# Performance work log

Hardware: AMD Instinct MI355X
Metric: run time of the kernel (lower is better)

Reference implementation:

```python
import jax, jax.numpy as jnp
import numpy as np


def setup_inputs() -> dict:
    key = jax.random.key(0)
    k1, k2, k3, k4 = jax.random.split(key, 4)
    B, S, E, A = 4, 4096, 1024, 1024
    embedded = jax.random.normal(k1, (B, S, E), dtype=jnp.float32)
    # nn.Linear(E, A, bias=False) weights, stored as [E, A] so y = x @ W
    Wk = jax.random.normal(k2, (E, A), dtype=jnp.float32) * (E ** -0.5)
    Wq = jax.random.normal(k3, (E, A), dtype=jnp.float32) * (E ** -0.5)
    Wv = jax.random.normal(k4, (E, A), dtype=jnp.float32) * (E ** -0.5)
    return {"embedded": embedded, "Wk": Wk, "Wq": Wq, "Wv": Wv}


def reference(embedded, Wk, Wq, Wv):
    # K, Q, V projections: [B, S, A]
    K = embedded @ Wk
    Q = embedded @ Wq
    V = embedded @ Wv
    A = K.shape[-1]
    S = embedded.shape[1]
    # causal scores [B, S, S]
    scores = jnp.einsum("bqa,bka->bqk", Q, K) / jnp.sqrt(jnp.float32(A))
    causal = jnp.tril(jnp.ones((S, S), dtype=bool))
    scores = jnp.where(causal, scores, -jnp.inf)
    probs = jax.nn.softmax(scores, axis=-1)
    out = jnp.einsum("bqk,bka->bqa", probs, V)
    # torch.round(out, decimals=4)
    return jnp.round(out, 4)
```

## Files before the change

### kernel.cpp

```cpp
#include <hip/hip_runtime.h>
#include <hip/hip_fp16.h>

typedef __attribute__((ext_vector_type(4))) float f32x4;
typedef __attribute__((ext_vector_type(8))) short s16x8;
typedef __attribute__((ext_vector_type(4))) short s16x4;
typedef unsigned short u16;
typedef unsigned int u32;

__device__ __forceinline__ u16 f2bf(float f) {
    union { float f; unsigned u; } x; x.f = f;
    return (u16)((x.u + 0x7fffu + ((x.u >> 16) & 1u)) >> 16);
}

__device__ __forceinline__ void ld16(const void* g, void* l) {
    __builtin_amdgcn_global_load_lds(
        (const __attribute__((address_space(1))) unsigned int*)g,
        (__attribute__((address_space(3))) unsigned int*)l, 16, 0, 0);
}

__device__ __forceinline__ void kstep64(const u16* gA, const u16* gB, const u16* gC,
                                        long lda, long ldb,
                                        u16* sA, u16* sB,
                                        int wm, int wn, int lm, int lg,
                                        f32x4 acc0[4][4], f32x4 acc1[4][4])
{
    const int t = threadIdx.x;
    __syncthreads();
#pragma unroll
    for (int p = 0; p < 4; p++) {
        ld16(gA + (long)p * 32 * lda, sA + p * 2048 + t * 8);
        ld16(gB + (long)p * 32 * ldb, sB + p * 2048 + t * 8);
        ld16(gC + (long)p * 32 * ldb, sB + 8192 + p * 2048 + t * 8);
    }
    __syncthreads();

#pragma unroll
    for (int s = 0; s < 2; s++) {
        s16x8 af[4], bf[4], cf[4];
        const int co = (((s * 4 + lg) ^ (lm & 7)) << 3);
#pragma unroll
        for (int i = 0; i < 4; i++) {
            af[i] = *(const s16x8*)&sA[(wm + i * 16 + lm) * 64 + co];
            bf[i] = *(const s16x8*)&sB[(wn + i * 16 + lm) * 64 + co];
            cf[i] = *(const s16x8*)&sB[8192 + (wn + i * 16 + lm) * 64 + co];
        }
#pragma unroll
        for (int i = 0; i < 4; i++)
#pragma unroll
            for (int j = 0; j < 4; j++) {
                acc0[i][j] = __builtin_amdgcn_mfma_f32_16x16x32_bf16(af[i], bf[j], acc0[i][j], 0, 0, 0);
                acc1[i][j] = __builtin_amdgcn_mfma_f32_16x16x32_bf16(af[i], cf[j], acc1[i][j], 0, 0, 0);
            }
    }
}

__device__ __forceinline__ void gemm_core64(const u16* A, long lda,
                                            const u16* B0, const u16* B1, long ldb,
                                            int m0, int kEnd,
                                            f32x4 acc0[4][4], f32x4 acc1[4][4],
                                            u16* sA, u16* sB)
{
    const int t    = threadIdx.x;
    const int lane = t & 63;
    const int wave = t >> 6;
    const int wm   = (wave & 1) << 6;
    const int wn   = (wave >> 1) << 6;
    const int lm   = lane & 15;
    const int lg   = lane >> 4;
    const int sr   = t >> 3;
    const int sc   = (((t & 7) ^ ((t >> 3) & 7)) << 3);
    const u16* gA0 = A + (long)(m0 + sr) * lda + sc;
    const u16* gB0 = B0 + (long)sr * ldb + sc;
    const u16* gC0 = B1 + (long)sr * ldb + sc;

    for (int k0 = 0; k0 < kEnd; k0 += 64)
        kstep64(gA0 + k0, gB0 + k0, gC0 + k0, lda, ldb,
                sA, sB, wm, wn, lm, lg, acc0, acc1);
}

__global__ void convert_x(const float* __restrict__ X, u16* __restrict__ Xb) {
    long idx = ((long)blockIdx.x * 256 + threadIdx.x) * 4;
    f32x4 v = *(const f32x4*)&X[idx];
    s16x4 o;
    o.x = (short)f2bf(v.x); o.y = (short)f2bf(v.y);
    o.z = (short)f2bf(v.z); o.w = (short)f2bf(v.w);
    *(s16x4*)&Xb[idx] = o;
}

__global__ void convert_w(const float* __restrict__ Wk, const float* __restrict__ Wq,
                          const float* __restrict__ Wv,
                          u16* __restrict__ Wkt, u16* __restrict__ Wqt, u16* __restrict__ Wvt) {
    const float* W; u16* O;
    if (blockIdx.y == 0)      { W = Wk; O = Wkt; }
    else if (blockIdx.y == 1) { W = Wq; O = Wqt; }
    else                      { W = Wv; O = Wvt; }
    __shared__ u16 tile[64][65];
    int k0 = (blockIdx.x >> 4) << 6, n0 = (blockIdx.x & 15) << 6;
    int t = threadIdx.x;
    int rr = t >> 4, cc = (t & 15) << 2;
#pragma unroll
    for (int i = 0; i < 4; i++) {
        int row = rr + i * 16;
        f32x4 v = *(const f32x4*)&W[(long)(k0 + row) * 1024 + n0 + cc];
        tile[row][cc + 0] = f2bf(v.x); tile[row][cc + 1] = f2bf(v.y);
        tile[row][cc + 2] = f2bf(v.z); tile[row][cc + 3] = f2bf(v.w);
    }
    __syncthreads();
#pragma unroll
    for (int i = 0; i < 4; i++) {
        int row = rr + i * 16;
        s16x4 pk;
        pk.x = (short)tile[cc + 0][row]; pk.y = (short)tile[cc + 1][row];
        pk.z = (short)tile[cc + 2][row]; pk.w = (short)tile[cc + 3][row];
        *(s16x4*)&O[(long)(n0 + row) * 1024 + k0 + cc] = pk;
    }
}

__global__ __launch_bounds__(256, 2) void proj_all(const u16* __restrict__ X,
                                                   const u16* __restrict__ Wqt,
                                                   const u16* __restrict__ Wkt,
                                                   const u16* __restrict__ Wvt,
                                                   u16* __restrict__ Qb,
                                                   u16* __restrict__ Kb,
                                                   u16* __restrict__ Vt) {
    __shared__ u16 sA[8192], sB[16384];
    int z   = blockIdx.x >> 9;
    int rem = blockIdx.x & 511;
    int m0  = (rem >> 2) * 128;
    int n0  = (rem & 3) * 256;
    const u16* Wt = (z == 0) ? Wqt : (z == 1) ? Wkt : Wvt;

    f32x4 acc0[4][4] = {}, acc1[4][4] = {};
    gemm_core64(X, 1024, Wt + (long)n0 * 1024, Wt + (long)(n0 + 128) * 1024, 1024,
                m0, 1024, acc0, acc1, sA, sB);

    int lane = threadIdx.x & 63, wave = threadIdx.x >> 6;
    int wm = (wave & 1) << 6, wn = (wave >> 1) << 6, lm = lane & 15, lg = lane >> 4;
    if (z < 2) {
        u16* O = (z == 0) ? Qb : Kb;
#pragma unroll
        for (int i = 0; i < 4; i++)
#pragma unroll
            for (int j = 0; j < 4; j++)
#pragma unroll
                for (int r = 0; r < 4; r++) {
                    int row = m0 + wm + i * 16 + lg * 4 + r;
                    int col = n0 + wn + j * 16 + lm;
                    O[(long)row * 1024 + col]       = f2bf(acc0[i][j][r]);
                    O[(long)row * 1024 + col + 128] = f2bf(acc1[i][j][r]);
                }
    } else {
#pragma unroll
        for (int i = 0; i < 4; i++)
#pragma unroll
            for (int j = 0; j < 4; j++) {
                int row0 = m0 + wm + i * 16 + lg * 4;
                int col  = n0 + wn + j * 16 + lm;
                int b = row0 >> 12, s = row0 & 4095;
                s16x4 p0, p1;
                p0.x = (short)f2bf(acc0[i][j][0]); p0.y = (short)f2bf(acc0[i][j][1]);
                p0.z = (short)f2bf(acc0[i][j][2]); p0.w = (short)f2bf(acc0[i][j][3]);
                p1.x = (short)f2bf(acc1[i][j][0]); p1.y = (short)f2bf(acc1[i][j][1]);
                p1.z = (short)f2bf(acc1[i][j][2]); p1.w = (short)f2bf(acc1[i][j][3]);
                *(s16x4*)&Vt[(long)b * 4194304 + (long)col * 4096 + s]         = p0;
                *(s16x4*)&Vt[(long)b * 4194304 + (long)(col + 128) * 4096 + s] = p1;
            }
    }
}

__global__ __launch_bounds__(256, 2) void sgemm_causal(const u16* __restrict__ Q,
                                                       const u16* __restrict__ K,
                                                       u16* __restrict__ S,
                                                       float* __restrict__ l) {
    __shared__ u16 sA[8192], sB[16384];
    int b  = blockIdx.x / 272;
    int tt = blockIdx.x % 272;
    int it = (int)(2.0f * sqrtf((float)tt + 1.0f)) - 1;
    if (it > 31) it = 31;
    if (it < 0) it = 0;
    while (it < 31 && (((it + 2) * (it + 2)) >> 2) <= tt) ++it;
    while (it > 0 && (((it + 1) * (it + 1)) >> 2) > tt) --it;
    int jp  = tt - (((it + 1) * (it + 1)) >> 2);
    int jt0 = jp * 2, jt1 = jt0 + 1;
    bool valid1 = (jt1 <= it);

    const u16* A  = Q + (long)b * 4194304;
    const u16* Kp = K + (long)b * 4194304;
    f32x4 acc0[4][4] = {}, acc1[4][4] = {};
    gemm_core64(A, 1024, Kp + (long)jt0 * 131072, Kp + (long)jt1 * 131072, 1024,
                it * 128, 1024, acc0, acc1, sA, sB);

    long tribase = (long)(b * 528 + ((it * (it + 1)) >> 1));
    u16* Sp0 = S + (tribase + jt0) * 16384;
    u16* Sp1 = S + (tribase + jt1) * 16384;
    int lane = threadIdx.x & 63, wave = threadIdx.x >> 6;
    int wm = (wave & 1) << 6, wn = (wave >> 1) << 6, lm = lane & 15, lg = lane >> 4;
    const float LOG2E = 1.44269504088896f;

    float rs[4][4];
#pragma unroll
    for (int i = 0; i < 4; i++)
#pragma unroll
        for (int r = 0; r < 4; r++) rs[i][r] = 0.0f;

#pragma unroll
    for (int i = 0; i < 4; i++)
#pragma unroll
        for (int j = 0; j < 4; j++)
#pragma unroll
            for (int r = 0; r < 4; r++) {
                int ri = wm + i * 16 + lg * 4 + r;
                int cj = wn + j * 16 + lm;
                int gi = it * 128 + ri;
                float p0 = (jt0 * 128 + cj > gi) ? 0.0f
                         : exp2f((acc0[i][j][r] * 0.03125f - 16.0f) * LOG2E);
                Sp0[ri * 128 + cj] = f2bf(p0);
                rs[i][r] += p0;
                if (valid1) {
                    float p1 = (jt1 * 128 + cj > gi) ? 0.0f
                             : exp2f((acc1[i][j][r] * 0.03125f - 16.0f) * LOG2E);
                    Sp1[ri * 128 + cj] = f2bf(p1);
                    rs[i][r] += p1;
                }
            }

#pragma unroll
    for (int i = 0; i < 4; i++)
#pragma unroll
        for (int r = 0; r < 4; r++) {
            float s = rs[i][r];
            s += __shfl_xor(s, 1, 64);
            s += __shfl_xor(s, 2, 64);
            s += __shfl_xor(s, 4, 64);
            s += __shfl_xor(s, 8, 64);
            if (lm == 0)
                atomicAdd(&l[b * 4096 + it * 128 + wm + i * 16 + lg * 4 + r], s);
        }
}

__global__ __launch_bounds__(256, 2) void pv_gemm(const u16* __restrict__ P,
                                                  const u16* __restrict__ Vt,
                                                  const float* __restrict__ l,
                                                  float* __restrict__ Out) {
    __shared__ u16 sA[8192], sB[16384];
    int g  = blockIdx.x;
    int it = (g < 256) ? (31 - (g >> 4)) : ((g - 256) >> 4);
    int rem = g & 15;
    int b   = rem >> 2;
    int atp = rem & 3;

    const int t    = threadIdx.x;
    const int lane = t & 63;
    const int wave = t >> 6;
    const int wm   = (wave & 1) << 6;
    const int wn   = (wave >> 1) << 6;
    const int lm   = lane & 15;
    const int lg   = lane >> 4;
    const int sr   = t >> 3;
    const int sc   = (((t & 7) ^ ((t >> 3) & 7)) << 3);

    const u16* Pbase = P + (long)(b * 528 + ((it * (it + 1)) >> 1)) * 16384;
    const u16* gA0 = Pbase + sr * 128 + sc;
    const u16* gB0 = Vt + (long)b * 4194304 + (long)(atp * 256 + sr) * 4096 + sc;
    const u16* gC0 = gB0 + (long)128 * 4096;

    f32x4 acc0[4][4] = {}, acc1[4][4] = {};
    for (int jt = 0; jt <= it; jt++) {
        long aoff = (long)jt * 16384;
        long boff = (long)jt * 128;
#pragma unroll
        for (int kk = 0; kk < 128; kk += 64)
            kstep64(gA0 + aoff + kk, gB0 + boff + kk, gC0 + boff + kk,
                    128, 4096, sA, sB, wm, wn, lm, lg, acc0, acc1);
    }

#pragma unroll
    for (int i = 0; i < 4; i++)
#pragma unroll
        for (int r = 0; r < 4; r++) {
            int gi = it * 128 + wm + i * 16 + lg * 4 + r;
            float scale = 1.0f / l[b * 4096 + gi];
#pragma unroll
            for (int j = 0; j < 4; j++) {
                int ga = atp * 256 + wn + j * 16 + lm;
                float* o = &Out[((long)b * 4096 + gi) * 1024 + ga];
                o[0]   = acc0[i][j][r] * scale;
                o[128] = acc1[i][j][r] * scale;
            }
        }
}

extern "C" void kernel_launch(void* const* d_in, const int* in_sizes, int n_in,
                              void* d_out, int out_size, void* d_ws, size_t ws_size,
                              hipStream_t stream) {
    const float* X  = (const float*)d_in[0];
    const float* Wk = (const float*)d_in[1];
    const float* Wq = (const float*)d_in[2];
    const float* Wv = (const float*)d_in[3];
    float* Out = (float*)d_out;

    char* w = (char*)d_ws;
    u16*   Qb   = (u16*)(w);
    u16*   Kb   = (u16*)(w + 33554432);
    u16*   Vt   = (u16*)(w + 67108864);
    float* l    = (float*)(w + 100663296);
    u16*   Xb   = (u16*)(w + 100728832);
    u16*   Wqt  = (u16*)(w + 134283264);
    u16*   Wkt  = (u16*)(w + 136380416);
    u16*   Wvt  = (u16*)(w + 138477568);
    u16*   S    = (u16*)(w + 100728832);

    hipMemsetAsync(l, 0, 65536, stream);
    convert_x<<<16384, 256, 0, stream>>>(X, Xb);
    convert_w<<<dim3(256, 3), 256, 0, stream>>>(Wk, Wq, Wv, Wkt, Wqt, Wvt);
    proj_all<<<1536, 256, 0, stream>>>(Xb, Wqt, Wkt, Wvt, Qb, Kb, Vt);
    sgemm_causal<<<1088, 256, 0, stream>>>(Qb, Kb, S, l);
    pv_gemm<<<512, 256, 0, stream>>>(S, Vt, l, Out);
}
```

Measured before the change: 433.4 us.

## Rewrite projection GEMM as 8-wave 256x256 tile with ping-pong LDS pipeline

Replaces the 4-wave 128x256 projection GEMM with an 8-wave kernel that computes 256x256 output tiles. It double-buffers A and B in LDS, using XOR-swizzled direct global-to-LDS loads, and interleaves quarter-tile MFMA phases with half-tile loads under explicit barriers, waitcnt fences and setprio. The goal is better data reuse per tile and overlap of global loads with matrix math. In exchange it uses 128KB of LDS per block and many barriers, which may limit occupancy, and correctness depends on the hand-tuned vmcnt accounting.

```diff
diff --git a/kernel.cpp b/kernel.cpp
--- a/kernel.cpp
+++ b/kernel.cpp
@@ -116,54 +116,163 @@
     }
 }
 
-__global__ __launch_bounds__(256, 2) void proj_all(const u16* __restrict__ X,
-                                                   const u16* __restrict__ Wqt,
-                                                   const u16* __restrict__ Wkt,
-                                                   const u16* __restrict__ Wvt,
-                                                   u16* __restrict__ Qb,
-                                                   u16* __restrict__ Kb,
-                                                   u16* __restrict__ Vt) {
-    __shared__ u16 sA[8192], sB[16384];
-    int z   = blockIdx.x >> 9;
-    int rem = blockIdx.x & 511;
-    int m0  = (rem >> 2) * 128;
-    int n0  = (rem & 3) * 256;
+__device__ __forceinline__ void stage_half64(const u16* gbase, u16* lbase,
+                                             int kt, int h, int t) {
+    const u16* g = gbase + (long)(h * 128) * 1024 + kt * 64;
+    u16* l = lbase + h * 8192 + t * 8;
+    ld16(g, l);
+    ld16(g + 64 * 1024, l + 4096);
+}
+
+__device__ __forceinline__ void read_A8(const u16* sA, int arow, int ih,
+                                        int co0, int co1, s16x8 af[4][2]) {
+#pragma unroll
+    for (int i = 0; i < 4; i++) {
+        af[i][0] = *(const s16x8*)&sA[(arow + (ih * 4 + i) * 16) * 64 + co0];
+        af[i][1] = *(const s16x8*)&sA[(arow + (ih * 4 + i) * 16) * 64 + co1];
+    }
+}
+
+__device__ __forceinline__ void read_B8(const u16* sB, int brow,
+                                        int co0, int co1, s16x8 bf[4][2]) {
+#pragma unroll
+    for (int j = 0; j < 4; j++) {
+        bf[j][0] = *(const s16x8*)&sB[(brow + j * 16) * 64 + co0];
+        bf[j][1] = *(const s16x8*)&sB[(brow + j * 16) * 64 + co1];
+    }
+}
+
+__device__ __forceinline__ void mfma16q(f32x4 acc[8][4], const s16x8 af[4][2],
+                                        const s16x8 bf[4][2], int ih, int jh) {
+    __builtin_amdgcn_s_setprio(1);
+#pragma unroll
+    for (int i = 0; i < 4; i++)
+#pragma unroll
+        for (int j = 0; j < 2; j++)
+#pragma unroll
+            for (int s = 0; s < 2; s++)
+                acc[ih * 4 + i][jh * 2 + j] = __builtin_amdgcn_mfma_f32_16x16x32_bf16(
+                    af[i][s], bf[jh * 2 + j][s], acc[ih * 4 + i][jh * 2 + j], 0, 0, 0);
+    __builtin_amdgcn_s_setprio(0);
+}
+
+#define PH_BAR()  __builtin_amdgcn_s_barrier()
+#define PH_LGKM() asm volatile("s_waitcnt lgkmcnt(0)" ::: "memory")
+
+__global__ __launch_bounds__(512, 2) void proj_all8(const u16* __restrict__ X,
+                                                    const u16* __restrict__ Wqt,
+                                                    const u16* __restrict__ Wkt,
+                                                    const u16* __restrict__ Wvt,
+                                                    u16* __restrict__ Qb,
+                                                    u16* __restrict__ Kb,
+                                                    u16* __restrict__ Vt) {
+    __shared__ u16 lds[65536];
+    const int bx  = blockIdx.x;
+    const int z   = bx >> 8;
+    const int rem = bx & 255;
+    const int m0  = (rem >> 2) << 8;
+    const int n0  = (rem & 3) << 8;
     const u16* Wt = (z == 0) ? Wqt : (z == 1) ? Wkt : Wvt;
 
-    f32x4 acc0[4][4] = {}, acc1[4][4] = {};
-    gemm_core64(X, 1024, Wt + (long)n0 * 1024, Wt + (long)(n0 + 128) * 1024, 1024,
-                m0, 1024, acc0, acc1, sA, sB);
-
-    int lane = threadIdx.x & 63, wave = threadIdx.x >> 6;
-    int wm = (wave & 1) << 6, wn = (wave >> 1) << 6, lm = lane & 15, lg = lane >> 4;
+    const int t  = threadIdx.x;
+    const int sr = t >> 3;
+    const int sc = ((t & 7) ^ (sr & 7)) << 3;
+    const u16* Ast = X  + (long)(m0 + sr) * 1024 + sc;
+    const u16* Bst = Wt + (long)(n0 + sr) * 1024 + sc;
+    u16* sA0 = lds;
+    u16* sA1 = lds + 16384;
+    u16* sB0 = lds + 32768;
+    u16* sB1 = lds + 49152;
+
+    const int lane = t & 63, w = t >> 6;
+    const int wr = w >> 2, wc = w & 3;
+    const int lm = lane & 15, lg = lane >> 4;
+    const int arow = wr * 128 + lm;
+    const int brow = wc * 64 + lm;
+    const int co0 = ((lg) ^ (lm & 7)) << 3;
+    const int co1 = ((4 + lg) ^ (lm & 7)) << 3;
+
+    f32x4 acc[8][4] = {};
+    s16x8 af[4][2], bf[4][2];
+
+    stage_half64(Bst, sB0, 0, 0, t); stage_half64(Bst, sB0, 0, 1, t);
+    stage_half64(Ast, sA0, 0, 0, t); stage_half64(Ast, sA0, 0, 1, t);
+    stage_half64(Bst, sB1, 1, 0, t); stage_half64(Bst, sB1, 1, 1, t);
+    stage_half64(Ast, sA1, 1, 0, t);
+    asm volatile("s_waitcnt vmcnt(6)" ::: "memory");
+    PH_BAR();
+
+#pragma unroll 1
+    for (int it = 0; it < 8; it++) {
+        const int  tO   = 2 * it + 1;
+        const bool more = (it < 7);
+        read_A8(sA0, arow, 0, co0, co1, af);
+        read_B8(sB0, brow, co0, co1, bf);
+        stage_half64(Ast, sA1, tO, 1, t);
+        PH_BAR(); PH_LGKM();
+        mfma16q(acc, af, bf, 0, 0);
+        PH_BAR();
+        if (more) stage_half64(Bst, sB0, tO + 1, 0, t);
+        PH_BAR(); PH_LGKM();
+        mfma16q(acc, af, bf, 0, 1);
+        PH_BAR();
+        read_A8(sA0, arow, 1, co0, co1, af);
+        if (more) stage_half64(Bst, sB0, tO + 1, 1, t);
+        PH_BAR(); PH_LGKM();
+        mfma16q(acc, af, bf, 1, 0);
+        PH_BAR();
+        if (more) stage_half64(Ast, sA0, tO + 1, 0, t);
+        PH_BAR(); PH_LGKM();
+        mfma16q(acc, af, bf, 1, 1);
+        if (more) asm volatile("s_waitcnt vmcnt(6)" ::: "memory");
+        else      asm volatile("s_waitcnt vmcnt(0)" ::: "memory");
+        PH_BAR();
+        read_A8(sA1, arow, 0, co0, co1, af);
+        read_B8(sB1, brow, co0, co1, bf);
+        if (more) stage_half64(Ast, sA0, tO + 1, 1, t);
+        PH_BAR(); PH_LGKM();
+        mfma16q(acc, af, bf, 0, 0);
+        PH_BAR();
+        if (more) stage_half64(Bst, sB1, tO + 2, 0, t);
+        PH_BAR(); PH_LGKM();
+        mfma16q(acc, af, bf, 0, 1);
+        PH_BAR();
+        read_A8(sA1, arow, 1, co0, co1, af);
+        if (more) stage_half64(Bst, sB1, tO + 2, 1, t);
+        PH_BAR(); PH_LGKM();
+        mfma16q(acc, af, bf, 1, 0);
+        PH_BAR();
+        if (more) stage_half64(Ast, sA1, tO + 2, 0, t);
+        PH_BAR(); PH_LGKM();
+        mfma16q(acc, af, bf, 1, 1);
+        if (more) asm volatile("s_waitcnt vmcnt(6)" ::: "memory");
+        PH_BAR();
+    }
+
     if (z < 2) {
         u16* O = (z == 0) ? Qb : Kb;
 #pragma unroll
-        for (int i = 0; i < 4; i++)
+        for (int i = 0; i < 8; i++)
 #pragma unroll
             for (int j = 0; j < 4; j++)
 #pragma unroll
                 for (int r = 0; r < 4; r++) {
-                    int row = m0 + wm + i * 16 + lg * 4 + r;
-                    int col = n0 + wn + j * 16 + lm;
-                    O[(long)row * 1024 + col]       = f2bf(acc0[i][j][r]);
-                    O[(long)row * 1024 + col + 128] = f2bf(acc1[i][j][r]);
+                    int row = m0 + wr * 128 + i * 16 + lg * 4 + r;
+                    int col = n0 + wc * 64 + j * 16 + lm;
+                    O[(long)row * 1024 + col] = f2bf(acc[i][j][r]);
                 }
     } else {
 #pragma unroll
-        for (int i = 0; i < 4; i++)
+        for (int i = 0; i < 8; i++)
 #pragma unroll
             for (int j = 0; j < 4; j++) {
-                int row0 = m0 + wm + i * 16 + lg * 4;
-                int col  = n0 + wn + j * 16 + lm;
+                int row0 = m0 + wr * 128 + i * 16 + lg * 4;
+                int col  = n0 + wc * 64 + j * 16 + lm;
                 int b = row0 >> 12, s = row0 & 4095;
-                s16x4 p0, p1;
-                p0.x = (short)f2bf(acc0[i][j][0]); p0.y = (short)f2bf(acc0[i][j][1]);
-                p0.z = (short)f2bf(acc0[i][j][2]); p0.w = (short)f2bf(acc0[i][j][3]);
-                p1.x = (short)f2bf(acc1[i][j][0]); p1.y = (short)f2bf(acc1[i][j][1]);
-                p1.z = (short)f2bf(acc1[i][j][2]); p1.w = (short)f2bf(acc1[i][j][3]);
-                *(s16x4*)&Vt[(long)b * 4194304 + (long)col * 4096 + s]         = p0;
-                *(s16x4*)&Vt[(long)b * 4194304 + (long)(col + 128) * 4096 + s] = p1;
+                s16x4 p0;
+                p0.x = (short)f2bf(acc[i][j][0]); p0.y = (short)f2bf(acc[i][j][1]);
+                p0.z = (short)f2bf(acc[i][j][2]); p0.w = (short)f2bf(acc[i][j][3]);
+                *(s16x4*)&Vt[(long)b * 4194304 + (long)col * 4096 + s] = p0;
             }
     }
 }
@@ -313,7 +422,7 @@
     hipMemsetAsync(l, 0, 65536, stream);
     convert_x<<<16384, 256, 0, stream>>>(X, Xb);
     convert_w<<<dim3(256, 3), 256, 0, stream>>>(Wk, Wq, Wv, Wkt, Wqt, Wvt);
-    proj_all<<<1536, 256, 0, stream>>>(Xb, Wqt, Wkt, Wvt, Qb, Kb, Vt);
+    proj_all8<<<768, 512, 0, stream>>>(Xb, Wqt, Wkt, Wvt, Qb, Kb, Vt);
     sgemm_causal<<<1088, 256, 0, stream>>>(Qb, Kb, S, l);
     pv_gemm<<<512, 256, 0, stream>>>(S, Vt, l, Out);
 }
```

Result: no change. 426.8 us (-1.5%).
